# Kernel tuning notes

Measured on AMD Instinct MI355X. Metric: run time of the kernel, lower is better.

The kernel has to match this reference:

```python
import jax, jax.numpy as jnp
import numpy as np

N_HEADS = 12   # config.n_heads; scores scaled by n_heads**-0.5 (faithful to source lambda)
TOPK = 128     # config.topk
K_SEEDS = 32   # config.k_seeds


def setup_inputs() -> dict:
    key = jax.random.key(0)
    k1, k2 = jax.random.split(key)
    B, N, H = 16, 8192, 768
    inp = jax.random.normal(k1, (B, N, H), dtype=jnp.float32)
    # seed param: xavier_uniform over (k_seeds, hidden) fan dims
    bound = float(np.sqrt(6.0 / (K_SEEDS + H)))
    seed = jax.random.uniform(k2, (1, K_SEEDS, H), minval=-bound, maxval=bound, dtype=jnp.float32)
    return {"input": inp, "seed": seed}


def reference(input, seed):
    # PMA pooling with top-k sparse attention (AttentionNoCache, causal_masking=False).
    # seed: [1, Q, H] broadcast to batch; input acts as both K and V: [B, N, H]
    B, N, H = input.shape
    q = jnp.broadcast_to(seed, (B,) + seed.shape[1:])            # [B, Q, H]
    scores = jnp.einsum('bqh,bnh->bqn', q, input)                # [B, Q, N]
    k = min(TOPK, N)
    vals, idx = jax.lax.top_k(scores, k)                         # [B, Q, k]
    # activation = dropout(softmax(x * n_heads**-0.5)); dropout is identity in eval
    attn = jax.nn.softmax(vals * (N_HEADS ** -0.5), axis=-1)     # [B, Q, k]
    # gather top-k values: V[b, idx[b,q,:], :] -> [B, Q, k, H]
    v = jnp.take_along_axis(input[:, None, :, :], idx[..., None], axis=2)
    return jnp.einsum('bqk,bqkh->bqh', attn, v)                  # [B, Q, H]
```

## Files before the change

### kernel.cpp

```cpp
#include <hip/hip_runtime.h>
#include <hip/hip_bf16.h>

constexpr int B = 16;
constexpr int N = 8192;
constexpr int H = 768;
constexpr int Q = 32;
constexpr int K = 128;
#define SCALE 0.28867513459481287f

typedef __attribute__((ext_vector_type(8))) short bf16x8_t;
typedef __attribute__((ext_vector_type(4))) float f32x4_t;

#define XS_OFF 0
#define XS_SPLIT 16384
#define SS_OFF 49152
#define SS_SPLIT 2048
#define LDS_BYTES 55296

__device__ __forceinline__ ushort f32_to_bf16_rn(float f) {
  uint32_t u = __float_as_uint(f);
  uint32_t r = (u + 0x7FFFu + ((u >> 16) & 1u)) >> 16;
  return (ushort)r;
}
__device__ __forceinline__ float bf16_to_f32(ushort h) {
  return __uint_as_float(((uint32_t)h) << 16);
}
__device__ __forceinline__ void split3(float f, ushort& h, ushort& m, ushort& l) {
  h = f32_to_bf16_rn(f);
  float f1 = f - bf16_to_f32(h);
  m = f32_to_bf16_rn(f1);
  float f2 = f1 - bf16_to_f32(m);
  l = f32_to_bf16_rn(f2);
}

__device__ __forceinline__ bf16x8_t ld_frag(const char* p, int row, int l4) {
  int sb = l4 ^ ((row >> 1) & 3);
  return *reinterpret_cast<const bf16x8_t*>(p + row * 64 + (sb << 4));
}

#define MFMA(a, b, c) __builtin_amdgcn_mfma_f32_16x16x32_bf16(a, b, c, 0, 0, 0)

#define STAGE_CHUNK(PX, PS)                                                    \
  {                                                                            \
    _Pragma("unroll") for (int r = 0; r < 4; ++r) {                            \
      const int row = sn + r * 64;                                             \
      const int byt = sh * 2;                                                  \
      const int sb = (byt >> 4) ^ ((row >> 1) & 3);                            \
      char* dst = lds + XS_OFF + row * 64 + (sb << 4) + (byt & 15);            \
      ushort4 uh, um, ul;                                                      \
      split3(PX[r].x, uh.x, um.x, ul.x);                                       \
      split3(PX[r].y, uh.y, um.y, ul.y);                                       \
      split3(PX[r].z, uh.z, um.z, ul.z);                                       \
      split3(PX[r].w, uh.w, um.w, ul.w);                                       \
      *reinterpret_cast<ushort4*>(dst + 0 * XS_SPLIT) = uh;                    \
      *reinterpret_cast<ushort4*>(dst + 1 * XS_SPLIT) = um;                    \
      *reinterpret_cast<ushort4*>(dst + 2 * XS_SPLIT) = ul;                    \
    }                                                                          \
    {                                                                          \
      const int byt = sh2 * 2;                                                 \
      const int sb = (byt >> 4) ^ ((sq >> 1) & 3);                             \
      char* dst = lds + SS_OFF + sq * 64 + (sb << 4) + (byt & 15);             \
      ushort2 uh, um, ul;                                                      \
      split3(PS.x, uh.x, um.x, ul.x);                                          \
      split3(PS.y, uh.y, um.y, ul.y);                                          \
      *reinterpret_cast<ushort2*>(dst + 0 * SS_SPLIT) = uh;                    \
      *reinterpret_cast<ushort2*>(dst + 1 * SS_SPLIT) = um;                    \
      *reinterpret_cast<ushort2*>(dst + 2 * SS_SPLIT) = ul;                    \
    }                                                                          \
  }

#define MFMA_CHUNK()                                                           \
  {                                                                            \
    const char* ssb = lds + SS_OFF;                                            \
    const char* xsb = lds + XS_OFF;                                            \
    bf16x8_t a0H = ld_frag(ssb + 0 * SS_SPLIT, l15, l4);                       \
    bf16x8_t a1H = ld_frag(ssb + 0 * SS_SPLIT, 16 + l15, l4);                  \
    bf16x8_t b0H = ld_frag(xsb + 0 * XS_SPLIT, nloc + l15, l4);                \
    bf16x8_t b1H = ld_frag(xsb + 0 * XS_SPLIT, nloc + 16 + l15, l4);           \
    bf16x8_t a0M = ld_frag(ssb + 1 * SS_SPLIT, l15, l4);                       \
    bf16x8_t a1M = ld_frag(ssb + 1 * SS_SPLIT, 16 + l15, l4);                  \
    bf16x8_t b0M = ld_frag(xsb + 1 * XS_SPLIT, nloc + l15, l4);                \
    bf16x8_t b1M = ld_frag(xsb + 1 * XS_SPLIT, nloc + 16 + l15, l4);           \
    bf16x8_t a0L = ld_frag(ssb + 2 * SS_SPLIT, l15, l4);                       \
    bf16x8_t a1L = ld_frag(ssb + 2 * SS_SPLIT, 16 + l15, l4);                  \
    bf16x8_t b0L = ld_frag(xsb + 2 * XS_SPLIT, nloc + l15, l4);                \
    bf16x8_t b1L = ld_frag(xsb + 2 * XS_SPLIT, nloc + 16 + l15, l4);           \
    acc00 = MFMA(a0H, b0H, acc00); acc01 = MFMA(a0H, b1H, acc01);              \
    acc10 = MFMA(a1H, b0H, acc10); acc11 = MFMA(a1H, b1H, acc11);              \
    acc00 = MFMA(a0H, b0M, acc00); acc01 = MFMA(a0H, b1M, acc01);              \
    acc10 = MFMA(a1H, b0M, acc10); acc11 = MFMA(a1H, b1M, acc11);              \
    acc00 = MFMA(a0M, b0H, acc00); acc01 = MFMA(a0M, b1H, acc01);              \
    acc10 = MFMA(a1M, b0H, acc10); acc11 = MFMA(a1M, b1H, acc11);              \
    acc00 = MFMA(a0M, b0M, acc00); acc01 = MFMA(a0M, b1M, acc01);              \
    acc10 = MFMA(a1M, b0M, acc10); acc11 = MFMA(a1M, b1M, acc11);              \
    acc00 = MFMA(a0H, b0L, acc00); acc01 = MFMA(a0H, b1L, acc01);              \
    acc10 = MFMA(a1H, b0L, acc10); acc11 = MFMA(a1H, b1L, acc11);              \
    acc00 = MFMA(a0L, b0H, acc00); acc01 = MFMA(a0L, b1H, acc01);              \
    acc10 = MFMA(a1L, b0H, acc10); acc11 = MFMA(a1L, b1H, acc11);              \
  }

__global__ __launch_bounds__(512, 4) void k_scores(const float* __restrict__ x,
                                                   const float* __restrict__ seed,
                                                   float* __restrict__ scores) {
  __shared__ __align__(16) char lds[LDS_BYTES];

  const int tid = threadIdx.x;
  const int bid = blockIdx.x;
  const int b = bid >> 5;
  const int nb = bid & 31;
  const size_t xbase = ((size_t)b * N + (size_t)nb * 256) * H;

  const int lane = tid & 63;
  const int wave = tid >> 6;
  const int l15 = lane & 15;
  const int l4 = lane >> 4;
  const int nloc = wave * 32;

  const int sn = tid >> 3;
  const int sh = (tid & 7) << 2;
  const int sq = tid >> 4;
  const int sh2 = (tid & 15) << 1;

  f32x4_t acc00 = {0.f, 0.f, 0.f, 0.f};
  f32x4_t acc01 = {0.f, 0.f, 0.f, 0.f};
  f32x4_t acc10 = {0.f, 0.f, 0.f, 0.f};
  f32x4_t acc11 = {0.f, 0.f, 0.f, 0.f};

  float4 pxA[4], pxB[4];
  float2 psA, psB;

  {
    const float* xp = x + xbase + sh;
#pragma unroll
    for (int r = 0; r < 4; ++r)
      pxA[r] = *reinterpret_cast<const float4*>(xp + (size_t)(sn + r * 64) * H);
    psA = *reinterpret_cast<const float2*>(seed + (size_t)sq * H + sh2);
  }

#pragma unroll 1
  for (int c = 0; c < 24; c += 2) {
    {
      const float* xp = x + xbase + (c + 1) * 32 + sh;
#pragma unroll
      for (int r = 0; r < 4; ++r)
        pxB[r] = *reinterpret_cast<const float4*>(xp + (size_t)(sn + r * 64) * H);
      psB = *reinterpret_cast<const float2*>(seed + (size_t)sq * H + (c + 1) * 32 + sh2);
    }
    STAGE_CHUNK(pxA, psA);
    __syncthreads();
    MFMA_CHUNK();
    __syncthreads();

    if (c + 2 < 24) {
      const float* xp = x + xbase + (c + 2) * 32 + sh;
#pragma unroll
      for (int r = 0; r < 4; ++r)
        pxA[r] = *reinterpret_cast<const float4*>(xp + (size_t)(sn + r * 64) * H);
      psA = *reinterpret_cast<const float2*>(seed + (size_t)sq * H + (c + 2) * 32 + sh2);
    }
    STAGE_CHUNK(pxB, psB);
    __syncthreads();
    MFMA_CHUNK();
    __syncthreads();
  }

  float* srow = scores + (((size_t)(b * Q)) << 13) + nb * 256 + nloc;
#pragma unroll
  for (int r = 0; r < 4; ++r) {
    srow[((size_t)(l4 * 4 + r) << 13) + l15] = acc00[r];
    srow[((size_t)(l4 * 4 + r) << 13) + 16 + l15] = acc01[r];
    srow[((size_t)(16 + l4 * 4 + r) << 13) + l15] = acc10[r];
    srow[((size_t)(16 + l4 * 4 + r) << 13) + 16 + l15] = acc11[r];
  }
}

__global__ __launch_bounds__(512) void k_topk(const float* __restrict__ scores,
                                              const float* __restrict__ x,
                                              float* __restrict__ out) {
  const int bq = blockIdx.x;
  const int b = bq >> 5;
  const int tid = threadIdx.x;
  const float* srow = scores + ((size_t)bq << 13);

  float f[16];
  uint32_t u[16];
  const float4* s4 = reinterpret_cast<const float4*>(srow);
#pragma unroll
  for (int i = 0; i < 4; ++i) {
    float4 v = s4[i * 512 + tid];
    f[i * 4 + 0] = v.x; f[i * 4 + 1] = v.y;
    f[i * 4 + 2] = v.z; f[i * 4 + 3] = v.w;
  }
#pragma unroll
  for (int e = 0; e < 16; ++e) {
    uint32_t bits = __float_as_uint(f[e]);
    u[e] = (bits & 0x80000000u) ? ~bits : (bits | 0x80000000u);
  }

  __shared__ int s_red[8];
  uint32_t lo = 0u, hi = 0xFFFFFFFFu;
  while (lo < hi) {
    uint32_t mid = lo + ((hi - lo) >> 1);
    int cnt = 0;
#pragma unroll
    for (int e = 0; e < 16; ++e) cnt += (u[e] > mid) ? 1 : 0;
#pragma unroll
    for (int m = 1; m < 64; m <<= 1) cnt += __shfl_xor(cnt, m);
    if ((tid & 63) == 0) s_red[tid >> 6] = cnt;
    __syncthreads();
    cnt = 0;
#pragma unroll
    for (int w = 0; w < 8; ++w) cnt += s_red[w];
    if (cnt >= K) lo = mid + 1; else hi = mid;
    __syncthreads();
  }
  const uint32_t T = lo;

  __shared__ int s_cnt, s_eqn;
  __shared__ int s_idx[K];
  __shared__ float s_w[K];
  __shared__ int s_eq[256];
  __shared__ float s_m, s_sum;
  if (tid == 0) { s_cnt = 0; s_eqn = 0; }
  __syncthreads();
#pragma unroll
  for (int e = 0; e < 16; ++e) {
    int n = (((e >> 2) * 512 + tid) << 2) + (e & 3);
    if (u[e] > T) {
      int p = atomicAdd(&s_cnt, 1);
      s_idx[p] = n;
      s_w[p] = f[e];
    } else if (u[e] == T) {
      int p = atomicAdd(&s_eqn, 1);
      if (p < 256) s_eq[p] = n;
    }
  }
  __syncthreads();
  const int c1 = s_cnt;
  const int need = K - c1;
  if (tid == 0 && need > 0) {
    uint32_t tb = (T & 0x80000000u) ? (T ^ 0x80000000u) : ~T;
    float tf = __uint_as_float(tb);
    int m = s_eqn; if (m > 256) m = 256;
    for (int a = 0; a < need; ++a) {
      int best = s_eq[a], bi = a;
      for (int z = a + 1; z < m; ++z)
        if (s_eq[z] < best) { best = s_eq[z]; bi = z; }
      s_eq[bi] = s_eq[a]; s_eq[a] = best;
      s_idx[c1 + a] = best;
      s_w[c1 + a] = tf;
    }
  }
  __syncthreads();

  if (tid < 64) {
    float v = fmaxf(s_w[tid], s_w[tid + 64]);
#pragma unroll
    for (int m = 1; m < 64; m <<= 1) v = fmaxf(v, __shfl_xor(v, m));
    if (tid == 0) s_m = v;
  }
  __syncthreads();
  const float mx = s_m * SCALE;
  if (tid < K) s_w[tid] = __expf(s_w[tid] * SCALE - mx);
  __syncthreads();
  if (tid < 64) {
    float v = s_w[tid] + s_w[tid + 64];
#pragma unroll
    for (int m = 1; m < 64; m <<= 1) v += __shfl_xor(v, m);
    if (tid == 0) s_sum = v;
  }
  __syncthreads();

  __shared__ __align__(16) float s_part[H];
  {
    const int t = tid & 255;
    const int ks = tid >> 8;
    float4 acc = make_float4(0.f, 0.f, 0.f, 0.f);
    if (t < 192) {
      const float4* xb =
          reinterpret_cast<const float4*>(x + (((size_t)b) << 13) * H);
      const int k0 = ks << 6;
#pragma unroll 4
      for (int k = k0; k < k0 + 64; ++k) {
        const float w = s_w[k];
        const float4 v = xb[(size_t)s_idx[k] * (H / 4) + t];
        acc.x = fmaf(w, v.x, acc.x);
        acc.y = fmaf(w, v.y, acc.y);
        acc.z = fmaf(w, v.z, acc.z);
        acc.w = fmaf(w, v.w, acc.w);
      }
    }
    if (ks == 0 && t < 192)
      reinterpret_cast<float4*>(s_part)[t] = acc;
    __syncthreads();
    if (ks == 1 && t < 192) {
      const float4 p = reinterpret_cast<const float4*>(s_part)[t];
      const float inv = 1.f / s_sum;
      float4 o;
      o.x = (acc.x + p.x) * inv;
      o.y = (acc.y + p.y) * inv;
      o.z = (acc.z + p.z) * inv;
      o.w = (acc.w + p.w) * inv;
      reinterpret_cast<float4*>(out)[(size_t)bq * (H / 4) + t] = o;
    }
  }
}

extern "C" void kernel_launch(void* const* d_in, const int* in_sizes, int n_in,
                              void* d_out, int out_size, void* d_ws, size_t ws_size,
                              hipStream_t stream) {
  const float* x = (const float*)d_in[0];
  const float* seed = (const float*)d_in[1];
  float* out = (float*)d_out;
  float* scores = (float*)d_ws;

  k_scores<<<512, 512, 0, stream>>>(x, seed, scores);
  k_topk<<<512, 512, 0, stream>>>(scores, x, out);
}
```

Before: 126.4 us.

## Load x fragments directly into registers and presplit seed in separate kernel

The scores kernel drops LDS staging and block barriers: each wave loads its x rows straight from global memory in MFMA fragment layout and splits them into bf16 hi/mid/lo in registers. Seed fragments are split once by a new small kernel into a scratch region of the output buffer and read directly by every wave. This aims to remove LDS write/read traffic, syncthreads stalls and redundant seed conversion, at the cost of less coalesced per-lane global loads and an extra launch.

```diff
diff --git a/kernel.cpp b/kernel.cpp
--- a/kernel.cpp
+++ b/kernel.cpp
@@ -11,80 +11,79 @@
 typedef __attribute__((ext_vector_type(8))) short bf16x8_t;
 typedef __attribute__((ext_vector_type(4))) float f32x4_t;
 
-#define XS_OFF 0
-#define XS_SPLIT 16384
-#define SS_OFF 49152
-#define SS_SPLIT 2048
-#define LDS_BYTES 55296
-
+__device__ __forceinline__ float bf16_to_f32(ushort h) {
+  return __uint_as_float(((uint32_t)h) << 16);
+}
 __device__ __forceinline__ ushort f32_to_bf16_rn(float f) {
   uint32_t u = __float_as_uint(f);
   uint32_t r = (u + 0x7FFFu + ((u >> 16) & 1u)) >> 16;
   return (ushort)r;
 }
-__device__ __forceinline__ float bf16_to_f32(ushort h) {
-  return __uint_as_float(((uint32_t)h) << 16);
-}
-__device__ __forceinline__ void split3(float f, ushort& h, ushort& m, ushort& l) {
+__device__ __forceinline__ void split3_rn(float f, ushort& h, ushort& m, ushort& l) {
   h = f32_to_bf16_rn(f);
   float f1 = f - bf16_to_f32(h);
   m = f32_to_bf16_rn(f1);
   float f2 = f1 - bf16_to_f32(m);
   l = f32_to_bf16_rn(f2);
 }
-
-__device__ __forceinline__ bf16x8_t ld_frag(const char* p, int row, int l4) {
-  int sb = l4 ^ ((row >> 1) & 3);
-  return *reinterpret_cast<const bf16x8_t*>(p + row * 64 + (sb << 4));
+__device__ __forceinline__ ushort cvt_bf16(float f) {
+  __hip_bfloat16 h = __float2bfloat16(f);
+  return __builtin_bit_cast(unsigned short, h);
+}
+__device__ __forceinline__ void split_row(const float4& a, const float4& b,
+                                          bf16x8_t& vh, bf16x8_t& vm, bf16x8_t& vl) {
+  const float f[8] = {a.x, a.y, a.z, a.w, b.x, b.y, b.z, b.w};
+#pragma unroll
+  for (int e = 0; e < 8; ++e) {
+    const float f0 = f[e];
+    const ushort h = cvt_bf16(f0);
+    const float r1 = f0 - bf16_to_f32(h);
+    const ushort m = cvt_bf16(r1);
+    const float r2 = r1 - bf16_to_f32(m);
+    const ushort l = cvt_bf16(r2);
+    vh[e] = (short)h; vm[e] = (short)m; vl[e] = (short)l;
+  }
 }
 
 #define MFMA(a, b, c) __builtin_amdgcn_mfma_f32_16x16x32_bf16(a, b, c, 0, 0, 0)
 
-#define STAGE_CHUNK(PX, PS)                                                    \
+__global__ void k_seedsplit(const float* __restrict__ seed,
+                            uint4* __restrict__ sfrag) {
+  const int c = blockIdx.x;
+  const int lane = threadIdx.x;
+  const int l15 = lane & 15;
+  const int l4 = lane >> 4;
+#pragma unroll
+  for (int t = 0; t < 2; ++t) {
+    const float* sp = seed + (size_t)(t * 16 + l15) * H + c * 32 + l4 * 8;
+    ushort uh[8], um[8], ul[8];
+#pragma unroll
+    for (int e = 0; e < 8; ++e) split3_rn(sp[e], uh[e], um[e], ul[e]);
+    uint4 rh, rm, rl;
+    rh.x = uh[0] | ((uint32_t)uh[1] << 16); rh.y = uh[2] | ((uint32_t)uh[3] << 16);
+    rh.z = uh[4] | ((uint32_t)uh[5] << 16); rh.w = uh[6] | ((uint32_t)uh[7] << 16);
+    rm.x = um[0] | ((uint32_t)um[1] << 16); rm.y = um[2] | ((uint32_t)um[3] << 16);
+    rm.z = um[4] | ((uint32_t)um[5] << 16); rm.w = um[6] | ((uint32_t)um[7] << 16);
+    rl.x = ul[0] | ((uint32_t)ul[1] << 16); rl.y = ul[2] | ((uint32_t)ul[3] << 16);
+    rl.z = ul[4] | ((uint32_t)ul[5] << 16); rl.w = ul[6] | ((uint32_t)ul[7] << 16);
+    sfrag[((c * 3 + 0) * 2 + t) * 64 + lane] = rh;
+    sfrag[((c * 3 + 1) * 2 + t) * 64 + lane] = rm;
+    sfrag[((c * 3 + 2) * 2 + t) * 64 + lane] = rl;
+  }
+}
+
+#define DO_CHUNK(C, PX0, PX1, PX2, PX3)                                        \
   {                                                                            \
-    _Pragma("unroll") for (int r = 0; r < 4; ++r) {                            \
-      const int row = sn + r * 64;                                             \
-      const int byt = sh * 2;                                                  \
-      const int sb = (byt >> 4) ^ ((row >> 1) & 3);                            \
-      char* dst = lds + XS_OFF + row * 64 + (sb << 4) + (byt & 15);            \
-      ushort4 uh, um, ul;                                                      \
-      split3(PX[r].x, uh.x, um.x, ul.x);                                       \
-      split3(PX[r].y, uh.y, um.y, ul.y);                                       \
-      split3(PX[r].z, uh.z, um.z, ul.z);                                       \
-      split3(PX[r].w, uh.w, um.w, ul.w);                                       \
-      *reinterpret_cast<ushort4*>(dst + 0 * XS_SPLIT) = uh;                    \
-      *reinterpret_cast<ushort4*>(dst + 1 * XS_SPLIT) = um;                    \
-      *reinterpret_cast<ushort4*>(dst + 2 * XS_SPLIT) = ul;                    \
-    }                                                                          \
-    {                                                                          \
-      const int byt = sh2 * 2;                                                 \
-      const int sb = (byt >> 4) ^ ((sq >> 1) & 3);                             \
-      char* dst = lds + SS_OFF + sq * 64 + (sb << 4) + (byt & 15);             \
-      ushort2 uh, um, ul;                                                      \
-      split3(PS.x, uh.x, um.x, ul.x);                                          \
-      split3(PS.y, uh.y, um.y, ul.y);                                          \
-      *reinterpret_cast<ushort2*>(dst + 0 * SS_SPLIT) = uh;                    \
-      *reinterpret_cast<ushort2*>(dst + 1 * SS_SPLIT) = um;                    \
-      *reinterpret_cast<ushort2*>(dst + 2 * SS_SPLIT) = ul;                    \
-    }                                                                          \
-  }
-
-#define MFMA_CHUNK()                                                           \
-  {                                                                            \
-    const char* ssb = lds + SS_OFF;                                            \
-    const char* xsb = lds + XS_OFF;                                            \
-    bf16x8_t a0H = ld_frag(ssb + 0 * SS_SPLIT, l15, l4);                       \
-    bf16x8_t a1H = ld_frag(ssb + 0 * SS_SPLIT, 16 + l15, l4);                  \
-    bf16x8_t b0H = ld_frag(xsb + 0 * XS_SPLIT, nloc + l15, l4);                \
-    bf16x8_t b1H = ld_frag(xsb + 0 * XS_SPLIT, nloc + 16 + l15, l4);           \
-    bf16x8_t a0M = ld_frag(ssb + 1 * SS_SPLIT, l15, l4);                       \
-    bf16x8_t a1M = ld_frag(ssb + 1 * SS_SPLIT, 16 + l15, l4);                  \
-    bf16x8_t b0M = ld_frag(xsb + 1 * XS_SPLIT, nloc + l15, l4);                \
-    bf16x8_t b1M = ld_frag(xsb + 1 * XS_SPLIT, nloc + 16 + l15, l4);           \
-    bf16x8_t a0L = ld_frag(ssb + 2 * SS_SPLIT, l15, l4);                       \
-    bf16x8_t a1L = ld_frag(ssb + 2 * SS_SPLIT, 16 + l15, l4);                  \
-    bf16x8_t b0L = ld_frag(xsb + 2 * XS_SPLIT, nloc + l15, l4);                \
-    bf16x8_t b1L = ld_frag(xsb + 2 * XS_SPLIT, nloc + 16 + l15, l4);           \
+    const int cb = (C) * 6;                                                    \
+    bf16x8_t a0H = __builtin_bit_cast(bf16x8_t, sfrag[(cb + 0) * 64 + lane]);  \
+    bf16x8_t a1H = __builtin_bit_cast(bf16x8_t, sfrag[(cb + 1) * 64 + lane]);  \
+    bf16x8_t a0M = __builtin_bit_cast(bf16x8_t, sfrag[(cb + 2) * 64 + lane]);  \
+    bf16x8_t a1M = __builtin_bit_cast(bf16x8_t, sfrag[(cb + 3) * 64 + lane]);  \
+    bf16x8_t a0L = __builtin_bit_cast(bf16x8_t, sfrag[(cb + 4) * 64 + lane]);  \
+    bf16x8_t a1L = __builtin_bit_cast(bf16x8_t, sfrag[(cb + 5) * 64 + lane]);  \
+    bf16x8_t b0H, b0M, b0L, b1H, b1M, b1L;                                     \
+    split_row(PX0, PX1, b0H, b0M, b0L);                                        \
+    split_row(PX2, PX3, b1H, b1M, b1L);                                        \
     acc00 = MFMA(a0H, b0H, acc00); acc01 = MFMA(a0H, b1H, acc01);              \
     acc10 = MFMA(a1H, b0H, acc10); acc11 = MFMA(a1H, b1H, acc11);              \
     acc00 = MFMA(a0H, b0M, acc00); acc01 = MFMA(a0H, b1M, acc01);              \
@@ -99,72 +98,51 @@
     acc10 = MFMA(a1L, b0H, acc10); acc11 = MFMA(a1L, b1H, acc11);              \
   }
 
-__global__ __launch_bounds__(512, 4) void k_scores(const float* __restrict__ x,
-                                                   const float* __restrict__ seed,
+__global__ __launch_bounds__(256, 3) void k_scores(const float* __restrict__ x,
+                                                   const uint4* __restrict__ sfrag,
                                                    float* __restrict__ scores) {
-  __shared__ __align__(16) char lds[LDS_BYTES];
-
-  const int tid = threadIdx.x;
-  const int bid = blockIdx.x;
-  const int b = bid >> 5;
-  const int nb = bid & 31;
-  const size_t xbase = ((size_t)b * N + (size_t)nb * 256) * H;
-
-  const int lane = tid & 63;
-  const int wave = tid >> 6;
+  const int gw = blockIdx.x * 4 + (threadIdx.x >> 6);
+  const int b = gw >> 8;
+  const int n0 = (gw & 255) * 32;
+  const int lane = threadIdx.x & 63;
   const int l15 = lane & 15;
   const int l4 = lane >> 4;
-  const int nloc = wave * 32;
-
-  const int sn = tid >> 3;
-  const int sh = (tid & 7) << 2;
-  const int sq = tid >> 4;
-  const int sh2 = (tid & 15) << 1;
+
+  const float* xr0 = x + ((size_t)b * N + n0 + l15) * H + l4 * 8;
+  const float* xr1 = xr0 + (size_t)16 * H;
 
   f32x4_t acc00 = {0.f, 0.f, 0.f, 0.f};
   f32x4_t acc01 = {0.f, 0.f, 0.f, 0.f};
   f32x4_t acc10 = {0.f, 0.f, 0.f, 0.f};
   f32x4_t acc11 = {0.f, 0.f, 0.f, 0.f};
 
-  float4 pxA[4], pxB[4];
-  float2 psA, psB;
-
-  {
-    const float* xp = x + xbase + sh;
-#pragma unroll
-    for (int r = 0; r < 4; ++r)
-      pxA[r] = *reinterpret_cast<const float4*>(xp + (size_t)(sn + r * 64) * H);
-    psA = *reinterpret_cast<const float2*>(seed + (size_t)sq * H + sh2);
-  }
+  float4 pA0, pA1, pA2, pA3, pB0, pB1, pB2, pB3;
+  pA0 = *reinterpret_cast<const float4*>(xr0);
+  pA1 = *reinterpret_cast<const float4*>(xr0 + 4);
+  pA2 = *reinterpret_cast<const float4*>(xr1);
+  pA3 = *reinterpret_cast<const float4*>(xr1 + 4);
 
 #pragma unroll 1
   for (int c = 0; c < 24; c += 2) {
     {
-      const float* xp = x + xbase + (c + 1) * 32 + sh;
-#pragma unroll
-      for (int r = 0; r < 4; ++r)
-        pxB[r] = *reinterpret_cast<const float4*>(xp + (size_t)(sn + r * 64) * H);
-      psB = *reinterpret_cast<const float2*>(seed + (size_t)sq * H + (c + 1) * 32 + sh2);
-    }
-    STAGE_CHUNK(pxA, psA);
-    __syncthreads();
-    MFMA_CHUNK();
-    __syncthreads();
-
+      const int o = (c + 1) * 32;
+      pB0 = *reinterpret_cast<const float4*>(xr0 + o);
+      pB1 = *reinterpret_cast<const float4*>(xr0 + o + 4);
+      pB2 = *reinterpret_cast<const float4*>(xr1 + o);
+      pB3 = *reinterpret_cast<const float4*>(xr1 + o + 4);
+    }
+    DO_CHUNK(c, pA0, pA1, pA2, pA3);
     if (c + 2 < 24) {
-      const float* xp = x + xbase + (c + 2) * 32 + sh;
-#pragma unroll
-      for (int r = 0; r < 4; ++r)
-        pxA[r] = *reinterpret_cast<const float4*>(xp + (size_t)(sn + r * 64) * H);
-      psA = *reinterpret_cast<const float2*>(seed + (size_t)sq * H + (c + 2) * 32 + sh2);
-    }
-    STAGE_CHUNK(pxB, psB);
-    __syncthreads();
-    MFMA_CHUNK();
-    __syncthreads();
-  }
-
-  float* srow = scores + (((size_t)(b * Q)) << 13) + nb * 256 + nloc;
+      const int o = (c + 2) * 32;
+      pA0 = *reinterpret_cast<const float4*>(xr0 + o);
+      pA1 = *reinterpret_cast<const float4*>(xr0 + o + 4);
+      pA2 = *reinterpret_cast<const float4*>(xr1 + o);
+      pA3 = *reinterpret_cast<const float4*>(xr1 + o + 4);
+    }
+    DO_CHUNK(c + 1, pB0, pB1, pB2, pB3);
+  }
+
+  float* srow = scores + (((size_t)(b * Q)) << 13) + n0;
 #pragma unroll
   for (int r = 0; r < 4; ++r) {
     srow[((size_t)(l4 * 4 + r) << 13) + l15] = acc00[r];
@@ -313,7 +291,9 @@
   const float* seed = (const float*)d_in[1];
   float* out = (float*)d_out;
   float* scores = (float*)d_ws;
-
-  k_scores<<<512, 512, 0, stream>>>(x, seed, scores);
+  uint4* sfrag = (uint4*)d_out;
+
+  k_seedsplit<<<24, 64, 0, stream>>>(seed, sfrag);
+  k_scores<<<1024, 256, 0, stream>>>(x, sfrag, scores);
   k_topk<<<512, 512, 0, stream>>>(scores, x, out);
 }
```

After: 150.7 us. 1.19x slower.
